# Kernel optimization log

Hardware: AMD Instinct MI355X
Metric: run time of the kernel (lower is better)

## Reference

```python
import jax, jax.numpy as jnp
import numpy as np

B, CIN, COUT, K, STRIDE, PAD = 32, 64, 128, 3, 1, 1
IN_H, IN_W = 112, 112


def setup_inputs() -> dict:
    key = jax.random.key(0)
    k1, k2 = jax.random.split(key)
    # x_padded already has `PAD` rows/cols of zeros on each side, as in the torch module
    x = jax.random.normal(k1, (B, CIN, IN_H, IN_W), dtype=jnp.float32)
    x_padded = jnp.pad(x, ((0, 0), (0, 0), (PAD, PAD), (PAD, PAD)))
    weight = jax.random.normal(k2, (COUT, CIN, K, K), dtype=jnp.float32) * 0.1
    bias = jnp.zeros((COUT,), dtype=jnp.float32)
    return {
        "x_padded": x_padded,
        "in_height": IN_H,
        "in_width": IN_W,
        "weight": weight,
        "bias": bias,
    }


def reference(x_padded, in_height, in_width, weight, bias):
    # CustomConv2D.custom_conv2d: direct conv over the pre-padded input.
    # out[b,o,h,w] = sum_{i,kh,kw} x_padded[b,i,h*s+kh,w*s+kw] * weight[o,i,kh,kw] + bias[o]
    out = jax.lax.conv_general_dilated(
        x_padded, weight,
        window_strides=(STRIDE, STRIDE),
        padding="VALID",  # padding already applied to x_padded
        dimension_numbers=("NCHW", "OIHW", "NCHW"),
    )
    return out + bias[None, :, None, None]
```

## Files before the change

### kernel.cpp

```cpp
#include <hip/hip_runtime.h>

typedef __attribute__((ext_vector_type(8))) short short8;
typedef __attribute__((ext_vector_type(4))) float f32x4;
typedef __attribute__((ext_vector_type(4))) unsigned int u32x4;
typedef unsigned short u16;
typedef unsigned int u32;

#define XH 114
#define XW 114
#define CINC 64
#define COUT 128
#define OH 112
#define OW 112
#define NB 32
#define KTOT 576
#define ROWB 14592

static __device__ __forceinline__ u16 f2bf(float f) {
    u32 x = __float_as_uint(f);
    u32 r = (x + 0x7fffu + ((x >> 16) & 1u)) >> 16;
    return (u16)r;
}

#define MFMA16(a, b, c) __builtin_amdgcn_mfma_f32_16x16x32_bf16((a), (b), (c), 0, 0, 0)

static __device__ __forceinline__ void gload16(const void* g, void* l) {
    __builtin_amdgcn_global_load_lds(
        (const __attribute__((address_space(1))) unsigned int*)g,
        (__attribute__((address_space(3))) unsigned int*)l, 16, 0, 0);
}


__global__ __launch_bounds__(256) void prep(const float* __restrict__ x,
                                            const float* __restrict__ w,
                                            u16* __restrict__ xb,
                                            u16* __restrict__ wbf) {
    const int tid = threadIdx.x;
    const int blk = blockIdx.x;
    if (blk >= NB * XH) {
        int i = (blk - NB * XH) * 256 + tid;
        int o = i / KTOT;
        int rem = i - o * KTOT;
        int khkw = rem >> 6;
        int ci = rem & 63;
        wbf[i] = f2bf(w[(o * CINC + ci) * 9 + khkw]);
        return;
    }
    __shared__ u16 tile[XW * 70];
    const int b = blk / XH;
    const int h = blk - b * XH;

    #pragma unroll
    for (int it = 0; it < 15; ++it) {
        int idx = it * 256 + tid;
        if (idx < 32 * XW) {
            int cp = idx / XW;
            int w_ = idx - cp * XW;
            const float* s0 = x + ((size_t)(b * CINC + 2 * cp) * XH + h) * XW + w_;
            float a = s0[0];
            float c = s0[XH * XW];
            u32 pk = (u32)f2bf(a) | ((u32)f2bf(c) << 16);
            *(u32*)&tile[w_ * 70 + 2 * cp] = pk;
        }
    }
    __syncthreads();

    u16* dstrow = xb + (size_t)(b * XH + h) * (XW * CINC);
    #pragma unroll
    for (int p2 = 0; p2 < 4; ++p2) {
        int task = p2 * 256 + tid;
        if (task < XW * 8) {
            int w_ = task >> 3;
            int c8 = task & 7;
            const u32* s = (const u32*)&tile[w_ * 70 + c8 * 8];
            u32x4 v = {s[0], s[1], s[2], s[3]};
            int slot = c8 ^ ((2 * h + w_) & 7);
            *(u32x4*)(dstrow + w_ * CINC + slot * 8) = v;
        }
    }
}

__global__ __launch_bounds__(256, 2) void conv_ring(const u16* __restrict__ xb,
                                                    const u16* __restrict__ wbf,
                                                    const float* __restrict__ bias,
                                                    float* __restrict__ out) {
    __shared__ u16 lds[4 * XW * CINC];
    char* ldsc = (char*)lds;

    const int tid  = threadIdx.x;
    const int lane = tid & 63;
    const int wv   = tid >> 6;
    const int l16  = lane & 15;
    const int lhi  = lane >> 4;

    int bidx = blockIdx.x;
    { int xcd = bidx & 7; bidx = xcd * 64 + (bidx >> 3); }
    const int bb = bidx >> 4;
    const int h0 = (bidx & 15) * 7;

    const u16* wrow0 = wbf + (wv * 32 + l16) * KTOT + lhi * 8;
    const u16* wrow1 = wrow0 + 16 * KTOT;
    short8 areg0[18], areg1[18];
    #pragma unroll
    for (int t = 0; t < 18; ++t) {
        areg0[t] = *(const short8*)(wrow0 + t * 32);
        areg1[t] = *(const short8*)(wrow1 + t * 32);
    }
    const float bv0 = bias[wv * 32 + l16];
    const float bv1 = bias[wv * 32 + 16 + l16];

    auto STAGE = [&](int hin) {
        const char* src = (const char*)(xb + (size_t)(bb * XH + hin) * (XW * CINC));
        char* dst = ldsc + (hin & 3) * ROWB;
        #pragma unroll
        for (int it = 0; it < 4; ++it) {
            const int c = it * 4 + wv;
            const int off = c * 1024;
            if (c < 14) {
                gload16(src + off + lane * 16, dst + off);
            } else if (c == 14) {
                if (lane < 16) gload16(src + off + lane * 16, dst + off);
            }
        }
    };

    STAGE(h0); STAGE(h0 + 1); STAGE(h0 + 2);
    __builtin_amdgcn_sched_barrier(0);
    asm volatile("s_waitcnt vmcnt(0) lgkmcnt(0)" ::: "memory");
    __builtin_amdgcn_sched_barrier(0);
    __builtin_amdgcn_s_barrier();

    const f32x4 zero = {0.f, 0.f, 0.f, 0.f};

    #pragma unroll 1
    for (int i = 0; i < 7; ++i) {
        const int hrow = h0 + i;
        if (i < 6) STAGE(hrow + 3);

        f32x4 acc[2][7];
        #pragma unroll
        for (int mf = 0; mf < 2; ++mf)
            #pragma unroll
            for (int nf = 0; nf < 7; ++nf) acc[mf][nf] = zero;

        #pragma unroll
        for (int tt = 0; tt < 9; ++tt) {
            const int kh = tt / 3;
            const int kw = tt - kh * 3;
            const int hin = hrow + kh;
            const int sb  = (hin & 3) * ROWB;
            const int hash = (2 * hin + kw + l16) & 7;
            const int ba0 = sb + ((kw + l16) << 7) + ((lhi ^ hash) << 4);

            #pragma unroll
            for (int nf = 0; nf < 7; ++nf) {
                short8 bf = *(const short8*)(ldsc + ba0 + nf * 2048);
                acc[0][nf] = MFMA16(bf, areg0[2 * tt], acc[0][nf]);
                acc[1][nf] = MFMA16(bf, areg1[2 * tt], acc[1][nf]);
            }
            #pragma unroll
            for (int nf = 0; nf < 7; ++nf) {
                short8 bf = *(const short8*)(ldsc + (ba0 ^ 0x40) + nf * 2048);
                acc[0][nf] = MFMA16(bf, areg0[2 * tt + 1], acc[0][nf]);
                acc[1][nf] = MFMA16(bf, areg1[2 * tt + 1], acc[1][nf]);
            }
        }

        #pragma unroll
        for (int mf = 0; mf < 2; ++mf) {
            const int o = wv * 32 + mf * 16 + l16;
            const float bv = mf ? bv1 : bv0;
            float* po = out + ((size_t)bb * COUT + o) * (OH * OW) + hrow * OW;
            #pragma unroll
            for (int nf = 0; nf < 7; ++nf) {
                f32x4 v = acc[mf][nf];
                v[0] += bv; v[1] += bv; v[2] += bv; v[3] += bv;
                *(f32x4*)(po + nf * 16 + lhi * 4) = v;
            }
        }

        __builtin_amdgcn_sched_barrier(0);
        asm volatile("s_waitcnt vmcnt(14) lgkmcnt(0)" ::: "memory");
        __builtin_amdgcn_sched_barrier(0);
        __builtin_amdgcn_s_barrier();
    }
}


#define BK 32
#define NSTEP 18
#define LDB 40

__global__ __launch_bounds__(256) void wcvt_ident(const float* __restrict__ w,
                                                  u16* __restrict__ wbf) {
    int i = blockIdx.x * 256 + threadIdx.x;
    if (i < COUT * KTOT) wbf[i] = f2bf(w[i]);
}

__global__ __launch_bounds__(256) void conv_fb(const float* __restrict__ x,
                                               const u16* __restrict__ wbf,
                                               const float* __restrict__ bias,
                                               float* __restrict__ out) {
    __shared__ u16 ldsB[OW * LDB];
    const int tid = threadIdx.x;
    int bid = blockIdx.x;
    { int xcd = bid & 7; bid = xcd * 448 + (bid >> 3); }
    const int b = bid / OH;
    const int h = bid - b * OH;
    const float* xbp = x + (size_t)b * (CINC * XH * XW);
    float* outb = out + (size_t)b * (COUT * OH * OW) + h * OW;
    const int lane = tid & 63, wv = tid >> 6, l16 = lane & 15, lhi = lane >> 4;
    const int m0 = wv * 32;
    const int sk = tid >> 3, sn0 = (tid & 7) * 14;
    f32x4 acc[2][7];
    const f32x4 zero = {0.f, 0.f, 0.f, 0.f};
    #pragma unroll
    for (int i = 0; i < 2; ++i)
        #pragma unroll
        for (int j = 0; j < 7; ++j) acc[i][j] = zero;
    for (int t = 0; t < NSTEP; ++t) {
        const int kg = t * BK + sk;
        const int ci = kg / 9;
        const int r9 = kg - ci * 9;
        const int kh = r9 / 3, kw = r9 - (r9 / 3) * 3;
        const float* src = xbp + ((size_t)ci * XH + (h + kh)) * XW + kw + sn0;
        __syncthreads();
        #pragma unroll
        for (int i = 0; i < 14; ++i) ldsB[(sn0 + i) * LDB + sk] = f2bf(src[i]);
        __syncthreads();
        short8 afrag[2];
        #pragma unroll
        for (int mf = 0; mf < 2; ++mf)
            afrag[mf] = *(const short8*)(wbf + (m0 + mf * 16 + l16) * KTOT + t * BK + lhi * 8);
        #pragma unroll
        for (int nf = 0; nf < 7; ++nf) {
            short8 bfrag = *(const short8*)&ldsB[(nf * 16 + l16) * LDB + lhi * 8];
            acc[0][nf] = MFMA16(afrag[0], bfrag, acc[0][nf]);
            acc[1][nf] = MFMA16(afrag[1], bfrag, acc[1][nf]);
        }
    }
    #pragma unroll
    for (int mf = 0; mf < 2; ++mf)
        #pragma unroll
        for (int j = 0; j < 4; ++j) {
            const int o = m0 + mf * 16 + lhi * 4 + j;
            const float bv = bias[o];
            #pragma unroll
            for (int nf = 0; nf < 7; ++nf)
                outb[(size_t)o * (OH * OW) + nf * 16 + l16] = acc[mf][nf][j] + bv;
        }
}

extern "C" void kernel_launch(void* const* d_in, const int* in_sizes, int n_in,
                              void* d_out, int out_size, void* d_ws, size_t ws_size,
                              hipStream_t stream) {
    const float* x    = (const float*)d_in[0];
    const float* w    = (const float*)d_in[3];
    const float* bias = (const float*)d_in[4];
    float* out = (float*)d_out;

    const size_t WBYTES = (size_t)COUT * KTOT * 2;
    const size_t XBYTES = (size_t)NB * XH * XW * CINC * 2;
    if (ws_size >= WBYTES + XBYTES) {
        u16* wbf = (u16*)d_ws;
        u16* xb  = (u16*)((char*)d_ws + WBYTES);
        prep<<<NB * XH + (COUT * KTOT) / 256, 256, 0, stream>>>(x, w, xb, wbf);
        conv_ring<<<512, 256, 0, stream>>>(xb, wbf, bias, out);
    } else {
        u16* wbf = (u16*)d_ws;
        wcvt_ident<<<(COUT * KTOT + 255) / 256, 256, 0, stream>>>(w, wbf);
        conv_fb<<<NB * OH, 256, 0, stream>>>(x, wbf, bias, out);
    }
}
```

Before: 110.5 us.

## Split conv block into 8 waves across output width, stream weights from memory

Doubles the block to 512 threads, so each 4-wave channel group now covers half of the output row (4 or 3 column fragments) instead of all 7. Weights are no longer kept in registers for the whole kernel; each wave reloads its A fragments from global/L2 on every kernel tap. This frees registers so more waves can be resident and latency is better hidden. The cost is repeated weight loads through the cache on every row and an uneven 4/3 split of column work between the two wave halves. The staging loop and vmcnt wait are adjusted to match the new wave count.

```diff
diff --git a/kernel.cpp b/kernel.cpp
--- a/kernel.cpp
+++ b/kernel.cpp
@@ -80,16 +80,19 @@
     }
 }
 
-__global__ __launch_bounds__(256, 2) void conv_ring(const u16* __restrict__ xb,
-                                                    const u16* __restrict__ wbf,
-                                                    const float* __restrict__ bias,
-                                                    float* __restrict__ out) {
+__global__ __launch_bounds__(512, 4) void conv_ring8(const u16* __restrict__ xb,
+                                                     const u16* __restrict__ wbf,
+                                                     const float* __restrict__ bias,
+                                                     float* __restrict__ out) {
     __shared__ u16 lds[4 * XW * CINC];
     char* ldsc = (char*)lds;
 
     const int tid  = threadIdx.x;
     const int lane = tid & 63;
     const int wv   = tid >> 6;
+    const int cg   = wv & 3;
+    const int ns   = wv >> 2;
+    const int nfn  = 4 - ns;
     const int l16  = lane & 15;
     const int lhi  = lane >> 4;
 
@@ -98,23 +101,17 @@
     const int bb = bidx >> 4;
     const int h0 = (bidx & 15) * 7;
 
-    const u16* wrow0 = wbf + (wv * 32 + l16) * KTOT + lhi * 8;
+    const u16* wrow0 = wbf + (cg * 32 + l16) * KTOT + lhi * 8;
     const u16* wrow1 = wrow0 + 16 * KTOT;
-    short8 areg0[18], areg1[18];
-    #pragma unroll
-    for (int t = 0; t < 18; ++t) {
-        areg0[t] = *(const short8*)(wrow0 + t * 32);
-        areg1[t] = *(const short8*)(wrow1 + t * 32);
-    }
-    const float bv0 = bias[wv * 32 + l16];
-    const float bv1 = bias[wv * 32 + 16 + l16];
+    const float bv0 = bias[cg * 32 + l16];
+    const float bv1 = bias[cg * 32 + 16 + l16];
 
     auto STAGE = [&](int hin) {
         const char* src = (const char*)(xb + (size_t)(bb * XH + hin) * (XW * CINC));
         char* dst = ldsc + (hin & 3) * ROWB;
         #pragma unroll
-        for (int it = 0; it < 4; ++it) {
-            const int c = it * 4 + wv;
+        for (int it = 0; it < 2; ++it) {
+            const int c = it * 8 + wv;
             const int off = c * 1024;
             if (c < 14) {
                 gload16(src + off + lane * 16, dst + off);
@@ -137,42 +134,50 @@
         const int hrow = h0 + i;
         if (i < 6) STAGE(hrow + 3);
 
-        f32x4 acc[2][7];
+        f32x4 acc[2][4];
         #pragma unroll
         for (int mf = 0; mf < 2; ++mf)
             #pragma unroll
-            for (int nf = 0; nf < 7; ++nf) acc[mf][nf] = zero;
-
-        #pragma unroll
-        for (int tt = 0; tt < 9; ++tt) {
-            const int kh = tt / 3;
-            const int kw = tt - kh * 3;
+            for (int nf = 0; nf < 4; ++nf) acc[mf][nf] = zero;
+
+        #pragma unroll
+        for (int kh = 0; kh < 3; ++kh) {
             const int hin = hrow + kh;
             const int sb  = (hin & 3) * ROWB;
-            const int hash = (2 * hin + kw + l16) & 7;
-            const int ba0 = sb + ((kw + l16) << 7) + ((lhi ^ hash) << 4);
-
-            #pragma unroll
-            for (int nf = 0; nf < 7; ++nf) {
-                short8 bf = *(const short8*)(ldsc + ba0 + nf * 2048);
-                acc[0][nf] = MFMA16(bf, areg0[2 * tt], acc[0][nf]);
-                acc[1][nf] = MFMA16(bf, areg1[2 * tt], acc[1][nf]);
+            #pragma unroll
+            for (int kw = 0; kw < 3; ++kw) {
+                const int tt = kh * 3 + kw;
+                const int hash = (2 * hin + kw + l16) & 7;
+                const int ba0 = sb + ((kw + ns * 64 + l16) << 7) + ((lhi ^ hash) << 4);
+                short8 a0 = *(const short8*)(wrow0 + 2 * tt * 32);
+                short8 a1 = *(const short8*)(wrow1 + 2 * tt * 32);
+                short8 a0b = *(const short8*)(wrow0 + (2 * tt + 1) * 32);
+                short8 a1b = *(const short8*)(wrow1 + (2 * tt + 1) * 32);
+                #pragma unroll
+                for (int nf = 0; nf < 4; ++nf) {
+                    if (nf >= nfn) break;
+                    short8 bf = *(const short8*)(ldsc + ba0 + nf * 2048);
+                    acc[0][nf] = MFMA16(bf, a0, acc[0][nf]);
+                    acc[1][nf] = MFMA16(bf, a1, acc[1][nf]);
+                }
+                #pragma unroll
+                for (int nf = 0; nf < 4; ++nf) {
+                    if (nf >= nfn) break;
+                    short8 bf = *(const short8*)(ldsc + (ba0 ^ 0x40) + nf * 2048);
+                    acc[0][nf] = MFMA16(bf, a0b, acc[0][nf]);
+                    acc[1][nf] = MFMA16(bf, a1b, acc[1][nf]);
+                }
             }
-            #pragma unroll
-            for (int nf = 0; nf < 7; ++nf) {
-                short8 bf = *(const short8*)(ldsc + (ba0 ^ 0x40) + nf * 2048);
-                acc[0][nf] = MFMA16(bf, areg0[2 * tt + 1], acc[0][nf]);
-                acc[1][nf] = MFMA16(bf, areg1[2 * tt + 1], acc[1][nf]);
-            }
         }
 
         #pragma unroll
         for (int mf = 0; mf < 2; ++mf) {
-            const int o = wv * 32 + mf * 16 + l16;
+            const int o = cg * 32 + mf * 16 + l16;
             const float bv = mf ? bv1 : bv0;
-            float* po = out + ((size_t)bb * COUT + o) * (OH * OW) + hrow * OW;
-            #pragma unroll
-            for (int nf = 0; nf < 7; ++nf) {
+            float* po = out + ((size_t)bb * COUT + o) * (OH * OW) + hrow * OW + ns * 64;
+            #pragma unroll
+            for (int nf = 0; nf < 4; ++nf) {
+                if (nf >= nfn) break;
                 f32x4 v = acc[mf][nf];
                 v[0] += bv; v[1] += bv; v[2] += bv; v[3] += bv;
                 *(f32x4*)(po + nf * 16 + lhi * 4) = v;
@@ -180,7 +185,7 @@
         }
 
         __builtin_amdgcn_sched_barrier(0);
-        asm volatile("s_waitcnt vmcnt(14) lgkmcnt(0)" ::: "memory");
+        asm volatile("s_waitcnt vmcnt(6) lgkmcnt(0)" ::: "memory");
         __builtin_amdgcn_sched_barrier(0);
         __builtin_amdgcn_s_barrier();
     }
@@ -265,7 +270,7 @@
         u16* wbf = (u16*)d_ws;
         u16* xb  = (u16*)((char*)d_ws + WBYTES);
         prep<<<NB * XH + (COUT * KTOT) / 256, 256, 0, stream>>>(x, w, xb, wbf);
-        conv_ring<<<512, 256, 0, stream>>>(xb, wbf, bias, out);
+        conv_ring8<<<512, 512, 0, stream>>>(xb, wbf, bias, out);
     } else {
         u16* wbf = (u16*)d_ws;
         wcvt_ident<<<(COUT * KTOT + 255) / 256, 256, 0, stream>>>(w, wbf);
```

After: 325.8 us. +195.0%, slower.
